# Performance work log

Hardware: AMD Instinct MI355X
Metric: run time of the kernel (lower is better)

## Reference

```python
import jax, jax.numpy as jnp
import numpy as np

BATCH = 1024
M = 64      # N_v measurements
N = 8192    # N_theta unknowns
STEPS = 3   # N_admm_steps
EPS_DIV = 1e-12


def setup_inputs() -> dict:
    key = jax.random.key(0)
    k = jax.random.split(key, 4)
    return {
        "r_n": jax.random.normal(k[0], (BATCH, 2, N), jnp.float32),
        "y": jax.random.normal(k[1], (BATCH, 2, M), jnp.float32),
        "u_in": jax.random.normal(k[2], (BATCH, 2, M), jnp.float32),
        "A": jax.random.normal(k[3], (2, M, N), jnp.float32) / np.sqrt(N).astype(np.float32),
        "log_rho": jnp.zeros((), jnp.float32),                 # rho = 1.0
        "log_epsilon": jnp.asarray(np.log(0.01), jnp.float32), # epsilon = 0.01
    }


def _cmm(Ar, Ai, v):
    # complex matmul A @ v : v [b,2,N] -> [b,2,M]
    vr, vi = v[:, 0], v[:, 1]
    return jnp.stack([vr @ Ar.T - vi @ Ai.T, vi @ Ar.T + vr @ Ai.T], axis=1)


def _chm(Ar, Ai, v):
    # complex conj-transpose matmul A^H @ v : v [b,2,M] -> [b,2,N]
    vr, vi = v[:, 0], v[:, 1]
    return jnp.stack([vr @ Ar + vi @ Ai, vi @ Ar - vr @ Ai], axis=1)


def reference(r_n, y, u_in, A, log_rho, log_epsilon):
    rho = jnp.exp(log_rho)
    epsilon = jnp.exp(log_epsilon)
    Ar, Ai = A[0], A[1]  # [M, N]

    # SMW system matrix: S = (1/rho) I + A A^H, written as real 2Mx2M block matrix.
    # It is constant across ADMM steps (rho fixed within a forward pass).
    I_M = jnp.eye(M, dtype=A.dtype)
    S_r = I_M / (rho + EPS_DIV) + Ar @ Ar.T + Ai @ Ai.T
    S_i = Ai @ Ar.T - Ar @ Ai.T
    S_block = jnp.block([[S_r, -S_i], [S_i, S_r]])  # [2M, 2M]

    x, z, u = r_n, y, u_in
    for _ in range(STEPS):
        # x-update via SMW: x = b - A^H (S^{-1} A b), b = r_n + rho A^H (z - u)
        b = r_n + rho * _chm(Ar, Ai, z - u)          # [b,2,N]
        Ab = _cmm(Ar, Ai, b)                          # [b,2,M]
        R = jnp.concatenate([Ab[:, 0], Ab[:, 1]], axis=1)  # [b,2M]
        sol = jnp.linalg.solve(S_block, R.T)          # [2M, b]
        T = jnp.stack([sol[:M].T, sol[M:].T], axis=1)  # [b,2,M]
        x = b - _chm(Ar, Ai, T)                       # [b,2,N]
        # enforce_real: zero imaginary part; enforce_positivity: clamp real part
        x = jnp.stack([jnp.maximum(x[:, 0], 0.0), jnp.zeros_like(x[:, 0])], axis=1)
        # z-update: project residual onto complex L2 ball of radius epsilon
        Ax = _cmm(Ar, Ai, x)                          # [b,2,M]
        v = Ax + u - y
        nrm = jnp.sqrt(jnp.sum(v * v, axis=(1, 2), keepdims=True))
        z = y + v * jnp.minimum(1.0, epsilon / (nrm + EPS_DIV))
        # dual update
        u = u + Ax - z
    return x, u
```

## Files before the change

### kernel.cpp

```cpp
#include <hip/hip_runtime.h>

#define B_ 1024
#define M_ 64
#define N_ 8192
#define NSG 16
#define NS3 8

typedef __attribute__((ext_vector_type(8))) short bf16x8;
typedef __attribute__((ext_vector_type(4))) float f32x4;

__device__ inline unsigned short f2b(float f) {
    union { float f; unsigned u; } v; v.f = f;
    unsigned r = v.u + 0x7FFFu + ((v.u >> 16) & 1u);
    return (unsigned short)(r >> 16);
}
__device__ inline unsigned rne2(float lo, float hi) {
    union { float f; unsigned u; } a, b; a.f = lo; b.f = hi;
    unsigned x = (a.u + 0x7FFFu + ((a.u >> 16) & 1u)) >> 16;
    unsigned y = (b.u + 0x7FFFu + ((b.u >> 16) & 1u)) >> 16;
    return x | (y << 16);
}
__device__ inline float rl(float v, int l) {
    return __builtin_bit_cast(float, __builtin_amdgcn_readlane(__builtin_bit_cast(int, v), l));
}

__global__ __launch_bounds__(256) void k_zero_imag(float* out) {
    int b = blockIdx.y;
    int n = (blockIdx.x * 256 + threadIdx.x) * 4;
    float4 z = make_float4(0.f, 0.f, 0.f, 0.f);
    *(float4*)(out + (size_t)(2 * b + 1) * N_ + n) = z;
}

__global__ __launch_bounds__(256) void k_cvt(const float* src, unsigned short* dst) {
    size_t i = ((size_t)blockIdx.x * 256 + threadIdx.x) * 8;
    float4 f0 = *(const float4*)(src + i);
    float4 f1 = *(const float4*)(src + i + 4);
    union { bf16x8 v; unsigned u[4]; } r;
    r.u[0] = rne2(f0.x, f0.y); r.u[1] = rne2(f0.z, f0.w);
    r.u[2] = rne2(f1.x, f1.y); r.u[3] = rne2(f1.z, f1.w);
    *(bf16x8*)(dst + i) = r.v;
}

__global__ __launch_bounds__(256) void k_prep_wg(const float* A, unsigned short* WgT) {
    int o = blockIdx.x;
    int kb = blockIdx.y * 2048 + threadIdx.x * 8;
    int m = o & 63;
    const float* Ar = A + (size_t)m * N_;
    const float* Ai = A + (size_t)M_ * N_ + (size_t)m * N_;
    bool oimag = o >= 64;
    bool khigh = kb >= N_;
    int koff = khigh ? kb - N_ : kb;
    const float* src = oimag ? (khigh ? Ar : Ai) : (khigh ? Ai : Ar);
    float sgn = (!oimag && khigh) ? -1.f : 1.f;
    float4 f0 = *(const float4*)(src + koff);
    float4 f1 = *(const float4*)(src + koff + 4);
    union { bf16x8 v; unsigned u[4]; } r;
    r.u[0] = rne2(sgn * f0.x, sgn * f0.y); r.u[1] = rne2(sgn * f0.z, sgn * f0.w);
    r.u[2] = rne2(sgn * f1.x, sgn * f1.y); r.u[3] = rne2(sgn * f1.z, sgn * f1.w);
    *(bf16x8*)(WgT + (size_t)o * 16384 + kb) = r.v;
}

__global__ __launch_bounds__(256) void k_transpA(const float* A, unsigned short* ATb) {
    __shared__ float tile[128][65];
    int n0 = blockIdx.x * 64;
    int t = threadIdx.x;
    int nl = t % 64, r0 = t / 64;
    for (int it = 0; it < 32; ++it) {
        int row = r0 + it * 4;
        tile[row][nl] = A[(size_t)row * N_ + n0 + nl];
    }
    __syncthreads();
    int o = t % 128, nn0 = t / 128;
    for (int it = 0; it < 32; ++it) {
        int nn = nn0 + it * 2;
        ATb[(size_t)(n0 + nn) * 128 + o] = f2b(tile[o][nn]);
    }
}

__global__ __launch_bounds__(256) void k_Sbuild(const float* A, const float* lr,
                                                float* S, float* AAHT) {
    __shared__ float redS[8];
    int bid = blockIdx.x;
    int i = 0, rem = bid;
    while (rem >= 64 - i) { rem -= 64 - i; ++i; }
    int j = i + rem;
    int t = threadIdx.x;
    const float* Ar = A;
    const float* Ai = A + (size_t)M_ * N_;
    const float* ari = Ar + (size_t)i * N_;
    const float* aii = Ai + (size_t)i * N_;
    const float* arj = Ar + (size_t)j * N_;
    const float* aij = Ai + (size_t)j * N_;
    float aR = 0.f, aI = 0.f;
#pragma unroll
    for (int it = 0; it < 8; ++it) {
        int n = it * 1024 + t * 4;
        float4 xr = *(const float4*)(ari + n);
        float4 xi = *(const float4*)(aii + n);
        float4 br = *(const float4*)(arj + n);
        float4 bi = *(const float4*)(aij + n);
        aR += xr.x * br.x + xi.x * bi.x + xr.y * br.y + xi.y * bi.y
            + xr.z * br.z + xi.z * bi.z + xr.w * br.w + xi.w * bi.w;
        aI += xi.x * br.x - xr.x * bi.x + xi.y * br.y - xr.y * bi.y
            + xi.z * br.z - xr.z * bi.z + xi.w * br.w - xr.w * bi.w;
    }
    for (int off = 32; off > 0; off >>= 1) {
        aR += __shfl_down(aR, off, 64);
        aI += __shfl_down(aI, off, 64);
    }
    int lane = t & 63, w = t >> 6;
    if (lane == 0) { redS[w * 2] = aR; redS[w * 2 + 1] = aI; }
    __syncthreads();
    if (t == 0) {
        float R = redS[0] + redS[2] + redS[4] + redS[6];
        float I = redS[1] + redS[3] + redS[5] + redS[7];
        float inv_rho = 1.0f / (expf(lr[0]) + 1e-12f);
        float diag = (i == j) ? inv_rho : 0.f;
        S[((size_t)i * 64 + j) * 2 + 0] = R + diag;
        S[((size_t)i * 64 + j) * 2 + 1] = I;
        AAHT[((size_t)j * 64 + i) * 2 + 0] = R;
        AAHT[((size_t)j * 64 + i) * 2 + 1] = I;
        if (i != j) {
            S[((size_t)j * 64 + i) * 2 + 0] = R;
            S[((size_t)j * 64 + i) * 2 + 1] = -I;
            AAHT[((size_t)i * 64 + j) * 2 + 0] = R;
            AAHT[((size_t)i * 64 + j) * 2 + 1] = -I;
        }
    }
}

__global__ __launch_bounds__(1024) void k_invert(const float* S, float* Wt) {
    __shared__ float2 fvs[2][64];
    int t = threadIdx.x;
    int lane = t & 63;
    int g = t >> 6;
    float mx0, my0, mx1, my1, mx2, my2, mx3, my3;
    float mx4, my4, mx5, my5, mx6, my6, mx7, my7;
#define GJ_INIT(J) { int c = 16 * (J) + g;                                   \
    if (c < 64) { float2 v = ((const float2*)S)[(size_t)lane * 64 + c];      \
                  mx##J = v.x; my##J = v.y; }                                \
    else { mx##J = (lane == c - 64) ? 1.f : 0.f; my##J = 0.f; } }
    GJ_INIT(0) GJ_INIT(1) GJ_INIT(2) GJ_INIT(3)
    GJ_INIT(4) GJ_INIT(5) GJ_INIT(6) GJ_INIT(7)
#undef GJ_INIT
    for (int k = 0; k < 64; ++k) {
        const int par = k & 1;
        if (g == (k & 15)) {
            switch (k >> 4) {
                case 0: fvs[par][lane] = make_float2(mx0, my0); break;
                case 1: fvs[par][lane] = make_float2(mx1, my1); break;
                case 2: fvs[par][lane] = make_float2(mx2, my2); break;
                default: fvs[par][lane] = make_float2(mx3, my3); break;
            }
        }
        __syncthreads();
        float2 f = fvs[par][lane];
        float2 p = fvs[par][k];
        float d = p.x * p.x + p.y * p.y;
        float id = 1.0f / d;
        float pix = p.x * id, piy = -p.y * id;
        bool isk = (lane == k);
        float a   = isk ? 0.f : 1.f;
        float fpx = isk ? -pix : (f.x * pix - f.y * piy);
        float fpy = isk ? -piy : (f.x * piy + f.y * pix);
#define GJ_UP(J) { float sx = rl(mx##J, k), sy = rl(my##J, k);               \
    float nx = a * mx##J - (fpx * sx - fpy * sy);                            \
    float ny = a * my##J - (fpx * sy + fpy * sx);                            \
    mx##J = nx; my##J = ny; }
        GJ_UP(0) GJ_UP(1) GJ_UP(2) GJ_UP(3)
        GJ_UP(4) GJ_UP(5) GJ_UP(6) GJ_UP(7)
#undef GJ_UP
    }
#define GJ_OUT(J) { int c = 16 * (J) + g;                                    \
    ((float2*)Wt)[(size_t)(c - 64) * 64 + lane] = make_float2(mx##J, my##J); }
    GJ_OUT(4) GJ_OUT(5) GJ_OUT(6) GJ_OUT(7)
#undef GJ_OUT
}

__global__ __launch_bounds__(256) void k_G(const unsigned short* rnb, const unsigned short* WgT,
                                           float* Gpart) {
    int t = threadIdx.x;
    int lane = t & 63;
    int w = t >> 6;
    int l15 = lane & 15;
    int q8 = (lane >> 4) * 8;
    int split = blockIdx.x;
    int b0 = blockIdx.y * 16;
    int k0 = split * 1024;
    f32x4 a00 = {}, a01 = {};
    const unsigned short* x0 = rnb + (size_t)(b0 + l15) * 16384 + k0 + q8;
    const unsigned short* w0 = WgT + (size_t)(w * 32 + l15) * 16384 + k0 + q8;
    const unsigned short* w1 = w0 + (size_t)16 * 16384;
#pragma unroll 8
    for (int ks = 0; ks < 32; ++ks) {
        int kk = ks * 32;
        bf16x8 af0 = *(const bf16x8*)(x0 + kk);
        bf16x8 bf0 = *(const bf16x8*)(w0 + kk);
        bf16x8 bf1 = *(const bf16x8*)(w1 + kk);
        a00 = __builtin_amdgcn_mfma_f32_16x16x32_bf16(af0, bf0, a00, 0, 0, 0);
        a01 = __builtin_amdgcn_mfma_f32_16x16x32_bf16(af0, bf1, a01, 0, 0, 0);
    }
    int row = (lane >> 4) * 4;
    size_t base = (size_t)split * (B_ * 128);
    float* g = Gpart + base + (size_t)(b0 + row) * 128 + w * 32 + l15;
#pragma unroll
    for (int r = 0; r < 4; ++r) {
        g[(size_t)r * 128] = a00[r];
        g[(size_t)r * 128 + 16] = a01[r];
    }
}

__global__ __launch_bounds__(256) void k_small12(const float* Gpart, const float* AAHT,
                                                 const float* Wt, const float* zin,
                                                 const float* uin, const float* lr,
                                                 unsigned short* qb) {
    __shared__ float2 AbS[4][64];
    int t = threadIdx.x;
    int m = t & 63;
    int w = __builtin_amdgcn_readfirstlane(t >> 6);
    int b = blockIdx.x * 4 + w;
    float rho = expf(lr[0]);
    float abR = 0.f, abI = 0.f;
    for (int k = 0; k < 64; ++k) {
        float wr = zin[(b * 2 + 0) * 64 + k] - uin[(b * 2 + 0) * 64 + k];
        float wi = zin[(b * 2 + 1) * 64 + k] - uin[(b * 2 + 1) * 64 + k];
        float2 h = *(const float2*)(AAHT + ((size_t)k * 64 + m) * 2);
        abR += wr * h.x - wi * h.y;
        abI += wi * h.x + wr * h.y;
    }
    float gR = 0.f, gI = 0.f;
#pragma unroll
    for (int s = 0; s < NSG; ++s) {
        gR += Gpart[(size_t)s * 131072 + (size_t)b * 128 + m];
        gI += Gpart[(size_t)s * 131072 + (size_t)b * 128 + 64 + m];
    }
    abR = gR + rho * abR;
    abI = gI + rho * abI;
    AbS[w][m] = make_float2(abR, abI);
    __syncthreads();
    float tR = 0.f, tI = 0.f;
    for (int k = 0; k < 64; ++k) {
        float2 Wv = *(const float2*)(Wt + ((size_t)k * 64 + m) * 2);
        float2 ab = AbS[w][k];
        tR += ab.x * Wv.x - ab.y * Wv.y;
        tI += ab.y * Wv.x + ab.x * Wv.y;
    }
    float wr_m = zin[(b * 2 + 0) * 64 + m] - uin[(b * 2 + 0) * 64 + m];
    float wi_m = zin[(b * 2 + 1) * 64 + m] - uin[(b * 2 + 1) * 64 + m];
    qb[(size_t)b * 128 + m] = f2b(rho * wr_m - tR);
    qb[(size_t)b * 128 + 64 + m] = f2b(rho * wi_m - tI);
}

__global__ __launch_bounds__(256, 3) void k_H23(const unsigned short* qb, const unsigned short* ATb,
                                                const float* rn, const unsigned short* Abf,
                                                float* out, float* Axpart, int last) {
    __shared__ __align__(16) char lds_buf[4 * 8448];
    int t = threadIdx.x;
    int lane = t & 63;
    int w = t >> 6;
    int l15 = lane & 15;
    int q8 = (lane >> 4) * 8;
    int row = (lane >> 4) * 4;
    int slab = blockIdx.x;
    int b0 = blockIdx.y * 16;
    int n0 = slab * 1024 + w * 256;
    short* xs = (short*)(lds_buf + w * 8448);
    float* rs = (float*)(lds_buf + w * 8448);

    bf16x8 a[4];
    const unsigned short* qrow = qb + (size_t)(b0 + l15) * 128 + q8;
#pragma unroll
    for (int ks = 0; ks < 4; ++ks) a[ks] = *(const bf16x8*)(qrow + ks * 32);
#pragma unroll 2
    for (int nt = 0; nt < 16; ++nt) {
        f32x4 acc = {};
        const unsigned short* bbase = ATb + (size_t)(n0 + nt * 16 + l15) * 128 + q8;
#pragma unroll
        for (int ks = 0; ks < 4; ++ks) {
            bf16x8 bf = *(const bf16x8*)(bbase + ks * 32);
            acc = __builtin_amdgcn_mfma_f32_16x16x32_bf16(a[ks], bf, acc, 0, 0, 0);
        }
        int ncol = n0 + nt * 16 + l15;
        int nloc = nt * 16 + l15;
#pragma unroll
        for (int r = 0; r < 4; ++r) {
            size_t ridx = (size_t)(b0 + row + r) * 16384 + ncol;
            float v = fmaxf(acc[r] + rn[ridx], 0.f);
            if (last) out[ridx] = v;
            xs[(row + r) * 264 + nloc] = (short)f2b(v);
        }
    }
    f32x4 acc8[8] = {};
#pragma unroll
    for (int ks = 0; ks < 8; ++ks) {
        bf16x8 xf = *(const bf16x8*)(xs + l15 * 264 + ks * 32 + q8);
#pragma unroll
        for (int ot = 0; ot < 8; ++ot) {
            const unsigned short* bp = Abf + (size_t)(ot * 16 + l15) * 8192 + n0 + ks * 32 + q8;
            acc8[ot] = __builtin_amdgcn_mfma_f32_16x16x32_bf16(xf, *(const bf16x8*)bp, acc8[ot], 0, 0, 0);
        }
    }
    __syncthreads();
#pragma unroll
    for (int ot = 0; ot < 8; ++ot)
#pragma unroll
        for (int r = 0; r < 4; ++r)
            rs[(row + r) * 132 + ot * 16 + l15] = acc8[ot][r];
    __syncthreads();
#pragma unroll
    for (int e = t; e < 2048; e += 256) {
        int b = e >> 7, o = e & 127;
        float sAx = 0.f;
#pragma unroll
        for (int ww = 0; ww < 4; ++ww)
            sAx += ((const float*)(lds_buf + ww * 8448))[b * 132 + o];
        Axpart[(size_t)slab * 131072 + (size_t)(b0 + b) * 128 + o] = sAx;
    }
}

__global__ __launch_bounds__(128) void k_small3(const float* Axpart, const float* uin,
                                                const float* y, const float* le,
                                                float* z, float* u, float* uout, int last) {
    __shared__ float red[2];
    int b = blockIdx.x, t = threadIdx.x;
    size_t idx = (size_t)b * 128 + t;
    float ax = 0.f;
#pragma unroll
    for (int s = 0; s < NS3; ++s) ax += Axpart[(size_t)s * 131072 + idx];
    float uo = uin[idx], yv = y[idx];
    float v = ax + uo - yv;
    float sq = v * v;
    for (int off = 32; off > 0; off >>= 1) sq += __shfl_down(sq, off, 64);
    if ((t & 63) == 0) red[t >> 6] = sq;
    __syncthreads();
    float tot = red[0] + red[1];
    float eps = expf(le[0]);
    float scale = fminf(1.f, eps / (sqrtf(tot) + 1e-12f));
    float zv = yv + v * scale;
    float un = uo + ax - zv;
    z[idx] = zv;
    u[idx] = un;
    if (last) uout[idx] = un;
}

extern "C" void kernel_launch(void* const* d_in, const int* in_sizes, int n_in,
                              void* d_out, int out_size, void* d_ws, size_t ws_size,
                              hipStream_t stream) {
    const float* rn  = (const float*)d_in[0];
    const float* y   = (const float*)d_in[1];
    const float* uin = (const float*)d_in[2];
    const float* A   = (const float*)d_in[3];
    const float* lr  = (const float*)d_in[4];
    const float* le  = (const float*)d_in[5];

    float* out = (float*)d_out;
    float* ws  = (float*)d_ws;

    float* Gpart  = ws;
    float* Axpart = Gpart + (size_t)NSG * 131072;
    float* S      = Axpart + (size_t)NS3 * 131072;
    float* AAHT   = S + 8192;
    float* Wt     = AAHT + 8192;
    float* z      = Wt + 8192;
    float* u      = z + 131072;
    unsigned short* qb  = (unsigned short*)(u + 131072);
    unsigned short* rnb = qb + 131072;
    unsigned short* WgT = rnb + (size_t)B_ * 16384;
    unsigned short* Abf = WgT + 2097152;
    unsigned short* ATb = Abf + 1048576;
    float* uout = out + (size_t)B_ * 2 * N_;

    k_zero_imag<<<dim3(8, B_), 256, 0, stream>>>(out);
    k_cvt<<<512, 256, 0, stream>>>(A, Abf);
    k_cvt<<<8192, 256, 0, stream>>>(rn, rnb);
    k_prep_wg<<<dim3(128, 8), 256, 0, stream>>>(A, WgT);
    k_transpA<<<128, 256, 0, stream>>>(A, ATb);
    k_Sbuild<<<2080, 256, 0, stream>>>(A, lr, S, AAHT);
    k_invert<<<1, 1024, 0, stream>>>(S, Wt);
    k_G<<<dim3(NSG, 64), 256, 0, stream>>>(rnb, WgT, Gpart);

    for (int step = 0; step < 3; ++step) {
        const float* zp = (step == 0) ? y   : z;
        const float* up = (step == 0) ? uin : u;
        int last = (step == 2) ? 1 : 0;
        k_small12<<<256, 256, 0, stream>>>(Gpart, AAHT, Wt, zp, up, lr, qb);
        k_H23<<<dim3(NS3, 64), 256, 0, stream>>>(qb, ATb, rn, Abf, out, Axpart, last);
        k_small3<<<B_, 128, 0, stream>>>(Axpart, up, y, le, z, u, uout, last);
    }
}
```

Baseline: 421.2 us.

## Fuse prep kernels, overlap inversion with G GEMM, read bf16 r_n in H23

Merges the A conversion, WgT build and transpose into one k_prep kernel that reads A once. The matrix inversion now runs as an extra block inside the G GEMM launch (k_Ginv), with 256 threads and a triangular skip of already-eliminated columns, so the serial inversion overlaps the GEMM. k_H23 reads r_n as bf16 instead of fp32 to cut memory traffic, and the imaginary-part zeroing moves into the last H23 step, removing a separate launch. The bf16 r_n read adds rounding error to the x-update, and the single inversion block may become a long tail.

```diff
diff --git a/kernel.cpp b/kernel.cpp
--- a/kernel.cpp
+++ b/kernel.cpp
@@ -20,15 +20,11 @@
     unsigned y = (b.u + 0x7FFFu + ((b.u >> 16) & 1u)) >> 16;
     return x | (y << 16);
 }
+__device__ inline float b2f(unsigned short s) {
+    union { unsigned u; float f; } v; v.u = ((unsigned)s) << 16; return v.f;
+}
 __device__ inline float rl(float v, int l) {
     return __builtin_bit_cast(float, __builtin_amdgcn_readlane(__builtin_bit_cast(int, v), l));
-}
-
-__global__ __launch_bounds__(256) void k_zero_imag(float* out) {
-    int b = blockIdx.y;
-    int n = (blockIdx.x * 256 + threadIdx.x) * 4;
-    float4 z = make_float4(0.f, 0.f, 0.f, 0.f);
-    *(float4*)(out + (size_t)(2 * b + 1) * N_ + n) = z;
 }
 
 __global__ __launch_bounds__(256) void k_cvt(const float* src, unsigned short* dst) {
@@ -41,36 +37,35 @@
     *(bf16x8*)(dst + i) = r.v;
 }
 
-__global__ __launch_bounds__(256) void k_prep_wg(const float* A, unsigned short* WgT) {
-    int o = blockIdx.x;
-    int kb = blockIdx.y * 2048 + threadIdx.x * 8;
-    int m = o & 63;
-    const float* Ar = A + (size_t)m * N_;
-    const float* Ai = A + (size_t)M_ * N_ + (size_t)m * N_;
-    bool oimag = o >= 64;
-    bool khigh = kb >= N_;
-    int koff = khigh ? kb - N_ : kb;
-    const float* src = oimag ? (khigh ? Ar : Ai) : (khigh ? Ai : Ar);
-    float sgn = (!oimag && khigh) ? -1.f : 1.f;
-    float4 f0 = *(const float4*)(src + koff);
-    float4 f1 = *(const float4*)(src + koff + 4);
-    union { bf16x8 v; unsigned u[4]; } r;
-    r.u[0] = rne2(sgn * f0.x, sgn * f0.y); r.u[1] = rne2(sgn * f0.z, sgn * f0.w);
-    r.u[2] = rne2(sgn * f1.x, sgn * f1.y); r.u[3] = rne2(sgn * f1.z, sgn * f1.w);
-    *(bf16x8*)(WgT + (size_t)o * 16384 + kb) = r.v;
-}
-
-__global__ __launch_bounds__(256) void k_transpA(const float* A, unsigned short* ATb) {
+__global__ __launch_bounds__(256) void k_prep(const float* A, unsigned short* Abf,
+                                              unsigned short* WgT, unsigned short* ATb) {
     __shared__ float tile[128][65];
     int n0 = blockIdx.x * 64;
     int t = threadIdx.x;
     int nl = t % 64, r0 = t / 64;
+#pragma unroll
     for (int it = 0; it < 32; ++it) {
         int row = r0 + it * 4;
         tile[row][nl] = A[(size_t)row * N_ + n0 + nl];
     }
     __syncthreads();
+#pragma unroll
+    for (int it = 0; it < 32; ++it) {
+        int row = r0 + it * 4;
+        float v = tile[row][nl];
+        unsigned short bv = f2b(v);
+        Abf[(size_t)row * N_ + n0 + nl] = bv;
+        if (row < 64) {
+            WgT[(size_t)row * 16384 + n0 + nl] = bv;
+            WgT[(size_t)(64 + row) * 16384 + 8192 + n0 + nl] = bv;
+        } else {
+            int m = row - 64;
+            WgT[(size_t)m * 16384 + 8192 + n0 + nl] = f2b(-v);
+            WgT[(size_t)(64 + m) * 16384 + n0 + nl] = bv;
+        }
+    }
     int o = t % 128, nn0 = t / 128;
+#pragma unroll
     for (int it = 0; it < 32; ++it) {
         int nn = nn0 + it * 2;
         ATb[(size_t)(n0 + nn) * 128 + o] = f2b(tile[o][nn]);
@@ -129,63 +124,83 @@
     }
 }
 
-__global__ __launch_bounds__(1024) void k_invert(const float* S, float* Wt) {
-    __shared__ float2 fvs[2][64];
+__global__ __launch_bounds__(256, 2) void k_Ginv(const unsigned short* rnb,
+                                                 const unsigned short* WgT,
+                                                 float* Gpart,
+                                                 const float* S, float* Wt) {
     int t = threadIdx.x;
     int lane = t & 63;
-    int g = t >> 6;
-    float mx0, my0, mx1, my1, mx2, my2, mx3, my3;
-    float mx4, my4, mx5, my5, mx6, my6, mx7, my7;
-#define GJ_INIT(J) { int c = 16 * (J) + g;                                   \
+    if (blockIdx.x == 1024) {
+        __shared__ float2 fvs[2][64];
+        int g = t >> 6;
+        float mx0,my0,mx1,my1,mx2,my2,mx3,my3,mx4,my4,mx5,my5,mx6,my6,mx7,my7;
+        float mx8,my8,mx9,my9,mx10,my10,mx11,my11,mx12,my12,mx13,my13,mx14,my14,mx15,my15;
+        float mx16,my16,mx17,my17,mx18,my18,mx19,my19,mx20,my20,mx21,my21,mx22,my22,mx23,my23;
+        float mx24,my24,mx25,my25,mx26,my26,mx27,my27,mx28,my28,mx29,my29,mx30,my30,mx31,my31;
+#define GJ_INIT(J) { int c = 4 * (J) + g;                                    \
     if (c < 64) { float2 v = ((const float2*)S)[(size_t)lane * 64 + c];      \
                   mx##J = v.x; my##J = v.y; }                                \
     else { mx##J = (lane == c - 64) ? 1.f : 0.f; my##J = 0.f; } }
-    GJ_INIT(0) GJ_INIT(1) GJ_INIT(2) GJ_INIT(3)
-    GJ_INIT(4) GJ_INIT(5) GJ_INIT(6) GJ_INIT(7)
+        GJ_INIT(0) GJ_INIT(1) GJ_INIT(2) GJ_INIT(3) GJ_INIT(4) GJ_INIT(5) GJ_INIT(6) GJ_INIT(7)
+        GJ_INIT(8) GJ_INIT(9) GJ_INIT(10) GJ_INIT(11) GJ_INIT(12) GJ_INIT(13) GJ_INIT(14) GJ_INIT(15)
+        GJ_INIT(16) GJ_INIT(17) GJ_INIT(18) GJ_INIT(19) GJ_INIT(20) GJ_INIT(21) GJ_INIT(22) GJ_INIT(23)
+        GJ_INIT(24) GJ_INIT(25) GJ_INIT(26) GJ_INIT(27) GJ_INIT(28) GJ_INIT(29) GJ_INIT(30) GJ_INIT(31)
 #undef GJ_INIT
-    for (int k = 0; k < 64; ++k) {
-        const int par = k & 1;
-        if (g == (k & 15)) {
-            switch (k >> 4) {
-                case 0: fvs[par][lane] = make_float2(mx0, my0); break;
-                case 1: fvs[par][lane] = make_float2(mx1, my1); break;
-                case 2: fvs[par][lane] = make_float2(mx2, my2); break;
-                default: fvs[par][lane] = make_float2(mx3, my3); break;
+        for (int k = 0; k < 64; ++k) {
+            const int par = k & 1;
+            if (g == (k & 3)) {
+                switch (k >> 2) {
+                    case 0:  fvs[par][lane] = make_float2(mx0,  my0);  break;
+                    case 1:  fvs[par][lane] = make_float2(mx1,  my1);  break;
+                    case 2:  fvs[par][lane] = make_float2(mx2,  my2);  break;
+                    case 3:  fvs[par][lane] = make_float2(mx3,  my3);  break;
+                    case 4:  fvs[par][lane] = make_float2(mx4,  my4);  break;
+                    case 5:  fvs[par][lane] = make_float2(mx5,  my5);  break;
+                    case 6:  fvs[par][lane] = make_float2(mx6,  my6);  break;
+                    case 7:  fvs[par][lane] = make_float2(mx7,  my7);  break;
+                    case 8:  fvs[par][lane] = make_float2(mx8,  my8);  break;
+                    case 9:  fvs[par][lane] = make_float2(mx9,  my9);  break;
+                    case 10: fvs[par][lane] = make_float2(mx10, my10); break;
+                    case 11: fvs[par][lane] = make_float2(mx11, my11); break;
+                    case 12: fvs[par][lane] = make_float2(mx12, my12); break;
+                    case 13: fvs[par][lane] = make_float2(mx13, my13); break;
+                    case 14: fvs[par][lane] = make_float2(mx14, my14); break;
+                    default: fvs[par][lane] = make_float2(mx15, my15); break;
+                }
             }
-        }
-        __syncthreads();
-        float2 f = fvs[par][lane];
-        float2 p = fvs[par][k];
-        float d = p.x * p.x + p.y * p.y;
-        float id = 1.0f / d;
-        float pix = p.x * id, piy = -p.y * id;
-        bool isk = (lane == k);
-        float a   = isk ? 0.f : 1.f;
-        float fpx = isk ? -pix : (f.x * pix - f.y * piy);
-        float fpy = isk ? -piy : (f.x * piy + f.y * pix);
-#define GJ_UP(J) { float sx = rl(mx##J, k), sy = rl(my##J, k);               \
+            __syncthreads();
+            float2 f = fvs[par][lane];
+            float2 p = fvs[par][k];
+            float d = p.x * p.x + p.y * p.y;
+            float id = 1.0f / d;
+            float pix = p.x * id, piy = -p.y * id;
+            bool isk = (lane == k);
+            float a   = isk ? 0.f : 1.f;
+            float fpx = isk ? -pix : (f.x * pix - f.y * piy);
+            float fpy = isk ? -piy : (f.x * piy + f.y * pix);
+#define GJ_UP(J) if (4 * (J) + g > k) {                                      \
+    float sx = rl(mx##J, k), sy = rl(my##J, k);                              \
     float nx = a * mx##J - (fpx * sx - fpy * sy);                            \
     float ny = a * my##J - (fpx * sy + fpy * sx);                            \
     mx##J = nx; my##J = ny; }
-        GJ_UP(0) GJ_UP(1) GJ_UP(2) GJ_UP(3)
-        GJ_UP(4) GJ_UP(5) GJ_UP(6) GJ_UP(7)
+            GJ_UP(0) GJ_UP(1) GJ_UP(2) GJ_UP(3) GJ_UP(4) GJ_UP(5) GJ_UP(6) GJ_UP(7)
+            GJ_UP(8) GJ_UP(9) GJ_UP(10) GJ_UP(11) GJ_UP(12) GJ_UP(13) GJ_UP(14) GJ_UP(15)
+            GJ_UP(16) GJ_UP(17) GJ_UP(18) GJ_UP(19) GJ_UP(20) GJ_UP(21) GJ_UP(22) GJ_UP(23)
+            GJ_UP(24) GJ_UP(25) GJ_UP(26) GJ_UP(27) GJ_UP(28) GJ_UP(29) GJ_UP(30) GJ_UP(31)
 #undef GJ_UP
-    }
-#define GJ_OUT(J) { int c = 16 * (J) + g;                                    \
+        }
+#define GJ_OUT(J) { int c = 4 * (J) + g;                                     \
     ((float2*)Wt)[(size_t)(c - 64) * 64 + lane] = make_float2(mx##J, my##J); }
-    GJ_OUT(4) GJ_OUT(5) GJ_OUT(6) GJ_OUT(7)
+        GJ_OUT(16) GJ_OUT(17) GJ_OUT(18) GJ_OUT(19) GJ_OUT(20) GJ_OUT(21) GJ_OUT(22) GJ_OUT(23)
+        GJ_OUT(24) GJ_OUT(25) GJ_OUT(26) GJ_OUT(27) GJ_OUT(28) GJ_OUT(29) GJ_OUT(30) GJ_OUT(31)
 #undef GJ_OUT
-}
-
-__global__ __launch_bounds__(256) void k_G(const unsigned short* rnb, const unsigned short* WgT,
-                                           float* Gpart) {
-    int t = threadIdx.x;
-    int lane = t & 63;
+        return;
+    }
     int w = t >> 6;
     int l15 = lane & 15;
     int q8 = (lane >> 4) * 8;
-    int split = blockIdx.x;
-    int b0 = blockIdx.y * 16;
+    int split = blockIdx.x & 15;
+    int b0 = (blockIdx.x >> 4) * 16;
     int k0 = split * 1024;
     f32x4 a00 = {}, a01 = {};
     const unsigned short* x0 = rnb + (size_t)(b0 + l15) * 16384 + k0 + q8;
@@ -252,7 +267,7 @@
 }
 
 __global__ __launch_bounds__(256, 3) void k_H23(const unsigned short* qb, const unsigned short* ATb,
-                                                const float* rn, const unsigned short* Abf,
+                                                const unsigned short* rnb, const unsigned short* Abf,
                                                 float* out, float* Axpart, int last) {
     __shared__ __align__(16) char lds_buf[4 * 8448];
     int t = threadIdx.x;
@@ -285,7 +300,7 @@
 #pragma unroll
         for (int r = 0; r < 4; ++r) {
             size_t ridx = (size_t)(b0 + row + r) * 16384 + ncol;
-            float v = fmaxf(acc[r] + rn[ridx], 0.f);
+            float v = fmaxf(acc[r] + b2f(rnb[ridx]), 0.f);
             if (last) out[ridx] = v;
             xs[(row + r) * 264 + nloc] = (short)f2b(v);
         }
@@ -315,6 +330,13 @@
         for (int ww = 0; ww < 4; ++ww)
             sAx += ((const float*)(lds_buf + ww * 8448))[b * 132 + o];
         Axpart[(size_t)slab * 131072 + (size_t)(b0 + b) * 128 + o] = sAx;
+    }
+    if (last) {
+        float4 z4 = make_float4(0.f, 0.f, 0.f, 0.f);
+        for (int e = t; e < 4096; e += 256) {
+            int bb = e >> 8, nq = e & 255;
+            *(float4*)(out + ((size_t)(b0 + bb) * 2 + 1) * N_ + slab * 1024 + nq * 4) = z4;
+        }
     }
 }
 
@@ -370,21 +392,17 @@
     unsigned short* ATb = Abf + 1048576;
     float* uout = out + (size_t)B_ * 2 * N_;
 
-    k_zero_imag<<<dim3(8, B_), 256, 0, stream>>>(out);
-    k_cvt<<<512, 256, 0, stream>>>(A, Abf);
+    k_prep<<<128, 256, 0, stream>>>(A, Abf, WgT, ATb);
     k_cvt<<<8192, 256, 0, stream>>>(rn, rnb);
-    k_prep_wg<<<dim3(128, 8), 256, 0, stream>>>(A, WgT);
-    k_transpA<<<128, 256, 0, stream>>>(A, ATb);
     k_Sbuild<<<2080, 256, 0, stream>>>(A, lr, S, AAHT);
-    k_invert<<<1, 1024, 0, stream>>>(S, Wt);
-    k_G<<<dim3(NSG, 64), 256, 0, stream>>>(rnb, WgT, Gpart);
+    k_Ginv<<<1025, 256, 0, stream>>>(rnb, WgT, Gpart, S, Wt);
 
     for (int step = 0; step < 3; ++step) {
         const float* zp = (step == 0) ? y   : z;
         const float* up = (step == 0) ? uin : u;
         int last = (step == 2) ? 1 : 0;
         k_small12<<<256, 256, 0, stream>>>(Gpart, AAHT, Wt, zp, up, lr, qb);
-        k_H23<<<dim3(NS3, 64), 256, 0, stream>>>(qb, ATb, rn, Abf, out, Axpart, last);
+        k_H23<<<dim3(NS3, 64), 256, 0, stream>>>(qb, ATb, rnb, Abf, out, Axpart, last);
         k_small3<<<B_, 128, 0, stream>>>(Axpart, up, y, le, z, u, uout, last);
     }
 }
```

New measurement: 409.0 us. -2.9%, faster.
